# Optimization experiments

Hardware: AMD Instinct MI355X
Metric: run time of the kernel (lower is better)

The kernel has to match this reference:

```python
import jax, jax.numpy as jnp
import numpy as np

# Adjacent1d: locally-connected 1D op with per-output-position unshared weights.
# out[b, oc, os] = sum_{ic, k} x[b, ic, start(os)+k] * W[ic, k, oc, os] + bias[oc, os]
# where start(os) = floor(os * in_s / out_s). With in_s = out_s * kernel_size the
# windows tile the input exactly (matches the assert in_s/kernel_size <= out_s).

B, IN_C, IN_S = 4, 64, 16384
OUT_C, OUT_S = 64, 4096
K = 4


def setup_inputs() -> dict:
    key = jax.random.key(0)
    k1, k2, k3 = jax.random.split(key, 3)
    x = jax.random.normal(k1, (B, IN_C, IN_S), dtype=jnp.float32)
    weights = jax.random.normal(k2, (IN_C, K, OUT_C, OUT_S), dtype=jnp.float32) * 0.05
    bias = jax.random.normal(k3, (OUT_C, OUT_S), dtype=jnp.float32) * 0.05
    return {"x": x, "weights": weights, "bias": bias}


def reference(x, weights, bias):
    in_s = x.shape[-1]
    out_s = weights.shape[-1]
    k = weights.shape[1]
    # window start per output position (proportional mapping)
    starts = (jnp.arange(out_s) * in_s) // out_s          # [out_s]
    idx = starts[:, None] + jnp.arange(k)[None, :]        # [out_s, K]
    idx = jnp.minimum(idx, in_s - 1)                      # safety clamp (no-op when in_s = out_s*K)
    gathered = x[:, :, idx]                               # [B, in_c, out_s, K]
    # contract over input channels and kernel taps with per-position weights
    out = jnp.einsum('bisk,ikos->bos', gathered, weights) # [B, out_c, out_s]
    return out + bias[None, :, :]
```

## Files before the change

### kernel.cpp

```cpp
#include <hip/hip_runtime.h>


__global__ __launch_bounds__(256) void adj1d_kernel(
    const float* __restrict__ x, const float* __restrict__ w,
    const float* __restrict__ bias, float* __restrict__ out) {

  int bid = blockIdx.x;
  int wgid = (bid & 7) * 64 + (bid >> 3);
  int og = wgid & 7;
  int st = wgid >> 3;
  int lane = threadIdx.x & 63;
  int wv   = threadIdx.x >> 6;
  int s  = (st << 6) + lane;
  int o0 = (og << 3) + (wv << 1);

  float acc00 = 0.f, acc01 = 0.f, acc02 = 0.f, acc03 = 0.f;
  float acc10 = 0.f, acc11 = 0.f, acc12 = 0.f, acc13 = 0.f;

  const float4* __restrict__ xv = reinterpret_cast<const float4*>(x);
  const float* __restrict__ wp0 = w + (o0 << 12) + s;

  #pragma unroll 2
  for (int i = 0; i < 64; ++i) {
    float xa[4][4];
    *reinterpret_cast<float4*>(xa[0]) = xv[((0 * 64 + i) << 12) + s];
    *reinterpret_cast<float4*>(xa[1]) = xv[((1 * 64 + i) << 12) + s];
    *reinterpret_cast<float4*>(xa[2]) = xv[((2 * 64 + i) << 12) + s];
    *reinterpret_cast<float4*>(xa[3]) = xv[((3 * 64 + i) << 12) + s];
    #pragma unroll
    for (int k = 0; k < 4; ++k) {
      const float* wp = wp0 + (size_t)(i * 4 + k) * 262144;
      float wa = wp[0];
      float wb = wp[4096];
      acc00 = fmaf(xa[0][k], wa, acc00);
      acc01 = fmaf(xa[1][k], wa, acc01);
      acc02 = fmaf(xa[2][k], wa, acc02);
      acc03 = fmaf(xa[3][k], wa, acc03);
      acc10 = fmaf(xa[0][k], wb, acc10);
      acc11 = fmaf(xa[1][k], wb, acc11);
      acc12 = fmaf(xa[2][k], wb, acc12);
      acc13 = fmaf(xa[3][k], wb, acc13);
    }
  }

  float bA = bias[(o0 << 12) + s];
  float bB = bias[((o0 + 1) << 12) + s];

  out[((0 * 64 + o0) << 12) + s]     = acc00 + bA;
  out[((1 * 64 + o0) << 12) + s]     = acc01 + bA;
  out[((2 * 64 + o0) << 12) + s]     = acc02 + bA;
  out[((3 * 64 + o0) << 12) + s]     = acc03 + bA;
  out[((0 * 64 + o0 + 1) << 12) + s] = acc10 + bB;
  out[((1 * 64 + o0 + 1) << 12) + s] = acc11 + bB;
  out[((2 * 64 + o0 + 1) << 12) + s] = acc12 + bB;
  out[((3 * 64 + o0 + 1) << 12) + s] = acc13 + bB;
}

extern "C" void kernel_launch(void* const* d_in, const int* in_sizes, int n_in,
                              void* d_out, int out_size, void* d_ws, size_t ws_size,
                              hipStream_t stream) {
  const float* x    = (const float*)d_in[0];
  const float* w    = (const float*)d_in[1];
  const float* bias = (const float*)d_in[2];
  float* out = (float*)d_out;

  adj1d_kernel<<<512, 256, 0, stream>>>(x, w, bias, out);
}
```

Baseline: 62.65 us.

## Software-pipeline input and weight loads four iterations ahead with register buffers

Restructures the input-channel loop into a four-stage register-buffered software pipeline: x and weight loads for channel i+4 are issued while the FMAs for channel i run. This raises the number of outstanding memory requests per thread to hide global-memory latency in a bandwidth-bound kernel. Launch bounds now request two blocks per CU, which caps registers even though the buffers raise register demand, so spilling is possible.

Measured after the change: 110.1 us. 75.8% more time.

```diff
diff --git a/kernel.cpp b/kernel.cpp
--- a/kernel.cpp
+++ b/kernel.cpp
@@ -1,7 +1,7 @@
 #include <hip/hip_runtime.h>
 
 
-__global__ __launch_bounds__(256) void adj1d_kernel(
+__global__ __launch_bounds__(256, 2) void adj1d_kernel(
     const float* __restrict__ x, const float* __restrict__ w,
     const float* __restrict__ bias, float* __restrict__ out) {
 
@@ -20,28 +20,53 @@
   const float4* __restrict__ xv = reinterpret_cast<const float4*>(x);
   const float* __restrict__ wp0 = w + (o0 << 12) + s;
 
-  #pragma unroll 2
-  for (int i = 0; i < 64; ++i) {
-    float xa[4][4];
-    *reinterpret_cast<float4*>(xa[0]) = xv[((0 * 64 + i) << 12) + s];
-    *reinterpret_cast<float4*>(xa[1]) = xv[((1 * 64 + i) << 12) + s];
-    *reinterpret_cast<float4*>(xa[2]) = xv[((2 * 64 + i) << 12) + s];
-    *reinterpret_cast<float4*>(xa[3]) = xv[((3 * 64 + i) << 12) + s];
-    #pragma unroll
-    for (int k = 0; k < 4; ++k) {
-      const float* wp = wp0 + (size_t)(i * 4 + k) * 262144;
-      float wa = wp[0];
-      float wb = wp[4096];
-      acc00 = fmaf(xa[0][k], wa, acc00);
-      acc01 = fmaf(xa[1][k], wa, acc01);
-      acc02 = fmaf(xa[2][k], wa, acc02);
-      acc03 = fmaf(xa[3][k], wa, acc03);
-      acc10 = fmaf(xa[0][k], wb, acc10);
-      acc11 = fmaf(xa[1][k], wb, acc11);
-      acc12 = fmaf(xa[2][k], wb, acc12);
-      acc13 = fmaf(xa[3][k], wb, acc13);
-    }
+  float4 xb[4][4];
+  float  wb[4][2][4];
+
+#define LOAD(p, i) do {                                                   \
+    xb[p][0] = xv[((0 * 64 + (i)) << 12) + s];                            \
+    xb[p][1] = xv[((1 * 64 + (i)) << 12) + s];                            \
+    xb[p][2] = xv[((2 * 64 + (i)) << 12) + s];                            \
+    xb[p][3] = xv[((3 * 64 + (i)) << 12) + s];                            \
+    const float* wp_ = wp0 + (size_t)(i) * 1048576;                       \
+    wb[p][0][0] = wp_[0];      wb[p][1][0] = wp_[4096];                   \
+    wb[p][0][1] = wp_[262144]; wb[p][1][1] = wp_[262144 + 4096];          \
+    wb[p][0][2] = wp_[524288]; wb[p][1][2] = wp_[524288 + 4096];          \
+    wb[p][0][3] = wp_[786432]; wb[p][1][3] = wp_[786432 + 4096];          \
+  } while (0)
+
+#define COMP(p) do {                                                      \
+    float xk0[4] = {xb[p][0].x, xb[p][0].y, xb[p][0].z, xb[p][0].w};      \
+    float xk1[4] = {xb[p][1].x, xb[p][1].y, xb[p][1].z, xb[p][1].w};      \
+    float xk2[4] = {xb[p][2].x, xb[p][2].y, xb[p][2].z, xb[p][2].w};      \
+    float xk3[4] = {xb[p][3].x, xb[p][3].y, xb[p][3].z, xb[p][3].w};      \
+    _Pragma("unroll")                                                     \
+    for (int k = 0; k < 4; ++k) {                                         \
+      float wa = wb[p][0][k], wc = wb[p][1][k];                           \
+      acc00 = fmaf(xk0[k], wa, acc00);                                    \
+      acc01 = fmaf(xk1[k], wa, acc01);                                    \
+      acc02 = fmaf(xk2[k], wa, acc02);                                    \
+      acc03 = fmaf(xk3[k], wa, acc03);                                    \
+      acc10 = fmaf(xk0[k], wc, acc10);                                    \
+      acc11 = fmaf(xk1[k], wc, acc11);                                    \
+      acc12 = fmaf(xk2[k], wc, acc12);                                    \
+      acc13 = fmaf(xk3[k], wc, acc13);                                    \
+    }                                                                     \
+  } while (0)
+
+  LOAD(0, 0); LOAD(1, 1); LOAD(2, 2); LOAD(3, 3);
+
+  #pragma unroll 1
+  for (int i = 0; i < 60; i += 4) {
+    COMP(0); LOAD(0, i + 4);
+    COMP(1); LOAD(1, i + 5);
+    COMP(2); LOAD(2, i + 6);
+    COMP(3); LOAD(3, i + 7);
   }
+  COMP(0); COMP(1); COMP(2); COMP(3);
+
+#undef LOAD
+#undef COMP
 
   float bA = bias[(o0 << 12) + s];
   float bB = bias[((o0 + 1) << 12) + s];
```
